# Performance work log

Measured on AMD Instinct MI355X. Metric: run time of the kernel, lower is better.

Reference implementation:

```python
import jax, jax.numpy as jnp
import numpy as np

B, T, E, HD, K, V = 128, 512, 128, 128, 20, 30000  # HD = hidden per direction


def _lstm_dir(x, Wih, Whh, b, reverse):
    # x: [T, B, D]; Wih: [4H, D]; Whh: [4H, H]; b: [4H] (b_ih + b_hh combined)
    if reverse:
        x = x[::-1]
    bsz = x.shape[1]
    xW = jnp.einsum('tbd,gd->tbg', x, Wih) + b  # [T, B, 4H] precompute input proj
    h0 = jnp.zeros((bsz, HD), x.dtype)
    c0 = jnp.zeros((bsz, HD), x.dtype)

    def step(carry, xw):
        h, c = carry
        z = xw + h @ Whh.T
        i, f, g, o = jnp.split(z, 4, axis=-1)  # PyTorch gate order i,f,g,o
        c = jax.nn.sigmoid(f) * c + jax.nn.sigmoid(i) * jnp.tanh(g)
        h = jax.nn.sigmoid(o) * jnp.tanh(c)
        return (h, c), h

    _, hs = jax.lax.scan(step, (h0, c0), xW)
    if reverse:
        hs = hs[::-1]
    return hs


def _bilstm_layer(x, Wih, Whh, b):
    # Wih/Whh: [2, 4H, D]/[2, 4H, H]; b: [2, 4H]
    hf = _lstm_dir(x, Wih[0], Whh[0], b[0], False)
    hb = _lstm_dir(x, Wih[1], Whh[1], b[1], True)
    return jnp.concatenate([hf, hb], axis=-1)  # [T, B, 2H]


def _crf_nll(emissions, tags, trans, start, end):
    # emissions: [B, T, K]; tags: [B, T]; full (all-ones) mask, reduction='mean'
    bsz = emissions.shape[0]
    em_tm = jnp.swapaxes(emissions, 0, 1)  # [T, B, K]
    tags_tm = tags.T                       # [T, B]
    bidx = jnp.arange(bsz)

    # --- numerator: path score ---
    score0 = start[tags_tm[0]] + em_tm[0][bidx, tags_tm[0]]

    def num_step(s, inp):
        em_t, tg_prev, tg_t = inp
        return s + trans[tg_prev, tg_t] + em_t[bidx, tg_t], None

    score, _ = jax.lax.scan(num_step, score0, (em_tm[1:], tags_tm[:-1], tags_tm[1:]))
    score = score + end[tags_tm[-1]]

    # --- denominator: forward algorithm (log partition) ---
    alpha0 = start[None, :] + em_tm[0]  # [B, K]

    def den_step(a, em_t):
        # a[b,i] + trans[i,j] + em_t[b,j] -> logsumexp over i
        a = jax.nn.logsumexp(a[:, :, None] + trans[None], axis=1) + em_t
        return a, None

    alpha, _ = jax.lax.scan(den_step, alpha0, em_tm[1:])
    logZ = jax.nn.logsumexp(alpha + end[None, :], axis=1)

    return -jnp.mean(score - logZ)


def setup_inputs() -> dict:
    key = jax.random.key(0)
    ks = jax.random.split(key, 16)
    u = lambda k, shape, s: jax.random.uniform(k, shape, jnp.float32, -s, s)
    kk = 1.0 / np.sqrt(HD)
    embed = jax.random.normal(ks[0], (V, E), jnp.float32) * 0.1
    embed = embed.at[0].set(0.0)  # padding_idx=0
    inp = {
        'sentences': jax.random.randint(ks[1], (B, T), 1, V),  # no pad tokens -> full mask
        'tags': jax.random.randint(ks[2], (B, T), 0, K),
        'lengths': jnp.full((B,), T, dtype=jnp.int64 if jax.config.jax_enable_x64 else jnp.int32),
        'embed': embed,
        'Wih0': u(ks[3], (2, 4 * HD, E), kk),
        'Whh0': u(ks[4], (2, 4 * HD, HD), kk),
        'b0': u(ks[5], (2, 4 * HD), kk),
        'Wih1': u(ks[6], (2, 4 * HD, 2 * HD), kk),
        'Whh1': u(ks[7], (2, 4 * HD, HD), kk),
        'b1': u(ks[8], (2, 4 * HD), kk),
        'Wout': u(ks[9], (K, 2 * HD), 1.0 / np.sqrt(2 * HD)),
        'bout': u(ks[10], (K,), 1.0 / np.sqrt(2 * HD)),
        'trans': u(ks[11], (K, K), 0.1),
        'start': u(ks[12], (K,), 0.1),
        'end': u(ks[13], (K,), 0.1),
    }
    return inp


def reference(sentences, tags, lengths, embed, Wih0, Whh0, b0, Wih1, Whh1, b1, Wout, bout, trans, start, end):
    # all lengths == T, so pack/pad is identity (eval-mode: no dropout)
    x = embed[sentences]                 # [B, T, E]
    x = jnp.swapaxes(x, 0, 1)            # [T, B, E] time-major for scan
    x = _bilstm_layer(x, Wih0, Whh0, b0)  # [T, B, 2H]
    x = _bilstm_layer(x, Wih1, Whh1, b1)  # [T, B, 2H]
    emissions = jnp.einsum('tbh,kh->tbk', x, Wout) + bout  # [T, B, K]
    emissions = jnp.swapaxes(emissions, 0, 1)              # [B, T, K]
    return _crf_nll(emissions, tags, trans, start, end)
```

## Files before the change

kernel.cpp:

```cpp
#include <hip/hip_runtime.h>
#include <hip/hip_bf16.h>
#include <cstddef>

typedef unsigned short u16;
typedef unsigned int u32;
typedef short bf16x8 __attribute__((ext_vector_type(8)));
typedef unsigned short u16x8 __attribute__((ext_vector_type(8)));
typedef float f32x4 __attribute__((ext_vector_type(4)));
typedef int i32x4 __attribute__((ext_vector_type(4)));
typedef int i32x8 __attribute__((ext_vector_type(8)));

constexpr int CB = 128;
constexpr int CT = 512;
constexpr int CE = 128;
constexpr int CK = 20;

constexpr size_t OFF_FLAG   = 0;
constexpr size_t OFF_WIH0   = 256;
constexpr size_t OFF_WHH0   = OFF_WIH0 + 262144;
constexpr size_t OFF_WIH1   = OFF_WHH0 + 262144;
constexpr size_t OFF_WHH1   = OFF_WIH1 + 524288;
constexpr size_t OFF_WOUT   = OFF_WHH1 + 262144;
constexpr size_t OFF_B0     = OFF_WOUT + 10240;
constexpr size_t OFF_B1     = OFF_B0 + 4096;
constexpr size_t OFF_BOUT   = OFF_B1 + 4096;
constexpr size_t OFF_TRANS  = OFF_BOUT + 256;
constexpr size_t OFF_START  = OFF_TRANS + 1792;
constexpr size_t OFF_END    = OFF_START + 256;
constexpr size_t OFF_PART   = OFF_END + 256;
constexpr size_t OFF_WHH0F8 = OFF_PART + 256;
constexpr size_t OFF_WHH1F8 = OFF_WHH0F8 + 131072;
constexpr size_t OFF_X0     = 2097152;
constexpr size_t OFF_H0     = OFF_X0 + 16777216;
constexpr size_t OFF_H1     = OFF_H0 + 33554432;
constexpr size_t OFF_EM     = OFF_H1 + 33554432;
constexpr size_t OFF_Z      = OFF_EM + 5242880;
constexpr size_t WS_NEED    = OFF_Z + 134217728;

__device__ __forceinline__ float b2f(u16 u) {
    union { u32 i; float f; } v; v.i = ((u32)u) << 16; return v.f;
}
__device__ __forceinline__ u16 f2b(float f) {
    union { float f; u32 i; } v; v.f = f;
    u32 r = v.i + 0x7FFFu + ((v.i >> 16) & 1u);
    return (u16)(r >> 16);
}
__device__ __forceinline__ float ldin(const void* p, long i, int bf) {
    return bf ? b2f(((const u16*)p)[i]) : ((const float*)p)[i];
}
__device__ __forceinline__ float sigm(float x) { return 1.0f / (1.0f + __expf(-x)); }
__device__ __forceinline__ float tanh_f(float x) { return 2.0f / (1.0f + __expf(-2.0f * x)) - 1.0f; }

__device__ __forceinline__ void gload_lds16(const void* g, void* l) {
    __builtin_amdgcn_global_load_lds(
        (const __attribute__((address_space(1))) void*)g,
        (__attribute__((address_space(3))) void*)l, 16, 0, 0);
}

__global__ void sniff_k(const unsigned char* __restrict__ traw, int* __restrict__ flag) {
    int lane = threadIdx.x;
    int votes = 0;
    for (int w = lane; w < 200; w += 64) {
        unsigned char b1 = traw[w * 4 + 1];
        unsigned char e = b1 & 0x7F;
        if (e >= 0x20 && e <= 0x3E) votes++;
    }
    #pragma unroll
    for (int off = 32; off; off >>= 1) votes += __shfl_xor(votes, off);
    if (lane == 0) *flag = (votes > 120) ? 1 : 0;
}

__global__ __launch_bounds__(256) void prep_k(
    const void* wih0, const void* whh0, const void* b0,
    const void* wih1, const void* whh1, const void* b1,
    const void* wout, const void* bout, const void* trans,
    const void* start, const void* end, unsigned char* ws)
{
    const int bf = *(const int*)(ws + OFF_FLAG);
    long tid = (long)blockIdx.x * 256 + threadIdx.x;
    u16* wih0b = (u16*)(ws + OFF_WIH0);
    u16* whh0b = (u16*)(ws + OFF_WHH0);
    u16* wih1b = (u16*)(ws + OFF_WIH1);
    u16* whh1b = (u16*)(ws + OFF_WHH1);
    u16* woutb = (u16*)(ws + OFF_WOUT);
    float* b0f   = (float*)(ws + OFF_B0);
    float* b1f   = (float*)(ws + OFF_B1);
    float* boutf = (float*)(ws + OFF_BOUT);
    float* trf   = (float*)(ws + OFF_TRANS);
    float* stf   = (float*)(ws + OFF_START);
    float* enf   = (float*)(ws + OFF_END);

    if (tid < 131072) { wih0b[tid] = f2b(ldin(wih0, tid, bf)); return; } tid -= 131072;
    if (tid < 131072) { whh0b[tid] = f2b(ldin(whh0, tid, bf)); return; } tid -= 131072;
    if (tid < 1024)   { b0f[tid]   = ldin(b0, tid, bf);        return; } tid -= 1024;
    if (tid < 262144) { wih1b[tid] = f2b(ldin(wih1, tid, bf)); return; } tid -= 262144;
    if (tid < 131072) { whh1b[tid] = f2b(ldin(whh1, tid, bf)); return; } tid -= 131072;
    if (tid < 1024)   { b1f[tid]   = ldin(b1, tid, bf);        return; } tid -= 1024;
    if (tid < 5120)   { woutb[tid] = f2b(ldin(wout, tid, bf)); return; } tid -= 5120;
    if (tid < 20)     { boutf[tid] = ldin(bout, tid, bf);      return; } tid -= 20;
    if (tid < 400)    { trf[tid]   = ldin(trans, tid, bf);     return; } tid -= 400;
    if (tid < 20)     { stf[tid]   = ldin(start, tid, bf);     return; } tid -= 20;
    if (tid < 20)     { enf[tid]   = ldin(end, tid, bf);       return; } tid -= 20;
    if (tid < 65536) {
        const float v0 = ldin(whh0, tid * 2, bf) * 8.0f;
        const float v1 = ldin(whh0, tid * 2 + 1, bf) * 8.0f;
        const u32 pk = __builtin_amdgcn_cvt_pk_fp8_f32(v0, v1, 0, false);
        ((u16*)(ws + OFF_WHH0F8))[tid] = (u16)(pk & 0xFFFF);
        return;
    } tid -= 65536;
    if (tid < 65536) {
        const float v0 = ldin(whh1, tid * 2, bf) * 8.0f;
        const float v1 = ldin(whh1, tid * 2 + 1, bf) * 8.0f;
        const u32 pk = __builtin_amdgcn_cvt_pk_fp8_f32(v0, v1, 0, false);
        ((u16*)(ws + OFF_WHH1F8))[tid] = (u16)(pk & 0xFFFF);
        return;
    }
}

__global__ __launch_bounds__(256) void gather_k(const void* __restrict__ embed,
                                                const int* __restrict__ sent,
                                                unsigned char* __restrict__ ws)
{
    const int bf = *(const int*)(ws + OFF_FLAG);
    u16* x0 = (u16*)(ws + OFF_X0);
    int tid = blockIdx.x * 256 + threadIdx.x;
    int m = tid >> 4, ch = tid & 15;
    int t = m >> 7, b = m & 127;
    int s = sent[b * CT + t];
    long src = (long)s * CE + ch * 8;
    u16x8 o;
    if (bf) {
        o = *(const u16x8*)((const u16*)embed + src);
    } else {
        const float* ef = (const float*)embed + src;
        f32x4 lo = *(const f32x4*)ef;
        f32x4 hi = *(const f32x4*)(ef + 4);
        o[0]=f2b(lo[0]); o[1]=f2b(lo[1]); o[2]=f2b(lo[2]); o[3]=f2b(lo[3]);
        o[4]=f2b(hi[0]); o[5]=f2b(hi[1]); o[6]=f2b(hi[2]); o[7]=f2b(hi[3]);
    }
    *(u16x8*)(x0 + (long)m * CE + ch * 8) = o;
}

template<int KD>
__global__ __launch_bounds__(256) void gemm_k(const u16* __restrict__ A,
                                              const u16* __restrict__ Bw,
                                              const float* __restrict__ bias,
                                              u16* __restrict__ Zp)
{
    const int bid = (blockIdx.x & 7) * 512 + (blockIdx.x >> 3);
    const int bm = bid >> 3, bn = bid & 7;
    const long m0 = (long)bm * 128;
    const int n0 = bn * 128;
    const int tid = threadIdx.x, lane = tid & 63, wave = tid >> 6;
    const int wm = wave >> 1, wn = wave & 1;
    const int lr = lane & 15, kg = (lane >> 4) * 8;

    __shared__ __align__(16) char smem[34816];
    __shared__ float bsm[128];
    u16 (*At)[64] = (u16(*)[64])smem;
    u16 (*Bt)[64] = (u16(*)[64])(smem + 16384);
    u16 (*cho)[136] = (u16(*)[136])smem;
    if (tid < 128) bsm[tid] = bias[n0 + tid];

    f32x4 acc[4][4];
    #pragma unroll
    for (int i = 0; i < 4; ++i)
        #pragma unroll
        for (int j = 0; j < 4; ++j) acc[i][j] = (f32x4){0.f, 0.f, 0.f, 0.f};

    const int srow = tid >> 3, scol = (tid & 7) * 8;
    char* db = smem + (tid & ~63) * 16;
    for (int kk = 0; kk < KD; kk += 64) {
        __syncthreads();
        #pragma unroll
        for (int r = 0; r < 4; ++r)
            gload_lds16(A + (m0 + srow + r * 32) * KD + kk + scol, db + r * 4096);
        #pragma unroll
        for (int r = 0; r < 4; ++r)
            gload_lds16(Bw + (long)(n0 + srow + r * 32) * KD + kk + scol,
                        db + 16384 + r * 4096);
        __syncthreads();
        #pragma unroll
        for (int kh = 0; kh < 64; kh += 32) {
            bf16x8 af[4], bfv[4];
            #pragma unroll
            for (int mt = 0; mt < 4; ++mt)
                af[mt] = *(const bf16x8*)&At[wm * 64 + mt * 16 + lr][kh + kg];
            #pragma unroll
            for (int nt = 0; nt < 4; ++nt)
                bfv[nt] = *(const bf16x8*)&Bt[wn * 64 + nt * 16 + lr][kh + kg];
            #pragma unroll
            for (int mt = 0; mt < 4; ++mt)
                #pragma unroll
                for (int nt = 0; nt < 4; ++nt)
                    acc[mt][nt] = __builtin_amdgcn_mfma_f32_16x16x32_bf16(
                        af[mt], bfv[nt], acc[mt][nt], 0, 0, 0);
        }
    }

    __syncthreads();
    const int rr0 = (lane >> 4) * 4;
    #pragma unroll
    for (int mt = 0; mt < 4; ++mt)
        #pragma unroll
        for (int nt = 0; nt < 4; ++nt) {
            const int colw = wn * 64 + nt * 16 + lr;
            const int pc = (colw >> 5) * 32 + ((colw & 15) << 1) + ((colw >> 4) & 1);
            const float bv = bsm[colw];
            #pragma unroll
            for (int r = 0; r < 4; ++r)
                cho[wm * 64 + mt * 16 + rr0 + r][pc] = f2b(acc[mt][nt][r] + bv);
        }
    __syncthreads();
    const int brow = tid >> 1, hf = tid & 1;
    const int dd = n0 >> 9, gt = (n0 >> 7) & 3;
    const int t = bm;
    const int sz = dd ? (CT - 1 - t) : t;
    u16* dst = Zp + ((long)sz * 256 + (brow * 2 + dd)) * 512 + gt * 128 + hf * 64;
    const u16* srcl = &cho[brow][hf * 64];
    #pragma unroll
    for (int p = 0; p < 8; ++p)
        *(u16x8*)(dst + p * 8) = *(const u16x8*)(srcl + p * 8);
}

__global__ __launch_bounds__(256, 1) void scan_k(const u16* __restrict__ Zp,
                                                 const unsigned char* __restrict__ Whh8,
                                                 u16* __restrict__ hout)
{
    const int b = blockIdx.x & 127, d = blockIdx.x >> 7;
    const int tid = threadIdx.x;
    const int lane = tid & 63;
    const int wave = tid >> 6;
    const int lr = lane & 15;
    const int kb8 = (lane >> 4) * 32;
    const int uhalf = (lane >> 4) & 1;
    const int rowm = wave * 32 + (lane & 31);

    i32x8 bfrag[4][2];
    #pragma unroll
    for (int gt = 0; gt < 4; ++gt)
        #pragma unroll
        for (int uu = 0; uu < 2; ++uu) {
            const unsigned char* wb = Whh8 +
                ((long)(d * 512 + gt * 128 + wave * 32 + uu * 16 + lr) << 7) + kb8;
            const i32x4 lo = *(const i32x4*)wb;
            const i32x4 hi = *(const i32x4*)(wb + 16);
            bfrag[gt][uu] = (i32x8){lo[0], lo[1], lo[2], lo[3], hi[0], hi[1], hi[2], hi[3]};
        }

    __shared__ __align__(16) unsigned char hbuf8[2 * 128];

    constexpr long SLAB = 256 * 256;
    const u32* zw0 = (const u32*)Zp + (long)(b * 2 + d) * 256 + wave * 16 + lr;

    u32 zR[16][4];
    #pragma unroll
    for (int s = 0; s < 16; ++s) {
        #pragma unroll
        for (int g = 0; g < 4; ++g)
            zR[s][g] = zw0[(long)s * SLAB + g * 64];
    }
    const u32* znext = zw0 + 16 * SLAB;

    if (tid < 128) { hbuf8[tid] = 0; hbuf8[128 + tid] = 0; }
    asm volatile("s_waitcnt lgkmcnt(0)\n\ts_barrier" ::: "memory");

    float cst = 0.f;
    u16* hp = hout + ((long)(d ? (CT - 1) : 0) * CB + b) * 256 + d * 128 + rowm;
    const long hstep = (long)(d ? -1 : 1) * (CB * 256);

    for (int grp = 0; grp < 32; ++grp) {
        const bool more = grp < 31;
        #pragma unroll
        for (int slot = 0; slot < 16; ++slot) {
            const u32 zl0 = zR[slot][0], zl1 = zR[slot][1];
            const u32 zl2 = zR[slot][2], zl3 = zR[slot][3];
            if (more) {
                const u32* zp = znext + (long)slot * SLAB;
                zR[slot][0] = zp[0];
                zR[slot][1] = zp[64];
                zR[slot][2] = zp[128];
                zR[slot][3] = zp[192];
            }

            const unsigned char* hbp = hbuf8 + (slot & 1) * 128 + kb8;
            const i32x4 hlo = *(const i32x4*)hbp;
            const i32x4 hhi = *(const i32x4*)(hbp + 16);
            const i32x8 av = (i32x8){hlo[0], hlo[1], hlo[2], hlo[3],
                                     hhi[0], hhi[1], hhi[2], hhi[3]};

            f32x4 acc[4][2];
            #pragma unroll
            for (int gt = 0; gt < 4; ++gt) {
                acc[gt][0] = (f32x4){0.f, 0.f, 0.f, 0.f};
                acc[gt][1] = (f32x4){0.f, 0.f, 0.f, 0.f};
            }
            #pragma unroll
            for (int gt = 0; gt < 4; ++gt) {
                acc[gt][0] = __builtin_amdgcn_mfma_scale_f32_16x16x128_f8f6f4(
                    av, bfrag[gt][0], acc[gt][0], 0, 0,
                    0, 0x7F7F7F7F, 0, 0x7F7F7F7F);
                acc[gt][1] = __builtin_amdgcn_mfma_scale_f32_16x16x128_f8f6f4(
                    av, bfrag[gt][1], acc[gt][1], 0, 0,
                    0, 0x7F7F7F7F, 0, 0x7F7F7F7F);
            }

            const u32 zlw[4] = {zl0, zl1, zl2, zl3};
            float pg[4];
            #pragma unroll
            for (int gt = 0; gt < 4; ++gt) {
                union { u32 i; float f; } zz;
                zz.i = uhalf ? (zlw[gt] & 0xFFFF0000u) : (zlw[gt] << 16);
                const float sv = uhalf ? acc[gt][1][0] : acc[gt][0][0];
                pg[gt] = fmaf(sv, 0.125f, zz.f);
            }
            const float iv = sigm(pg[0]);
            const float fv = sigm(pg[1]);
            const float gg = tanh_f(pg[2]);
            const float ov = sigm(pg[3]);
            cst = fmaf(fv, cst, iv * gg);
            const float h = ov * tanh_f(cst);

            if (lane < 32) {
                const u32 pk = __builtin_amdgcn_cvt_pk_fp8_f32(h, h, 0, false);
                hbuf8[((slot + 1) & 1) * 128 + rowm] = (unsigned char)(pk & 0xFF);
                *hp = f2b(h);
            }
            hp += hstep;
            asm volatile("s_waitcnt lgkmcnt(0)\n\ts_barrier" ::: "memory");
        }
        znext += 16 * SLAB;
    }
}

__global__ __launch_bounds__(256) void emis_k(const u16* __restrict__ h1,
                                              const u16* __restrict__ woutb,
                                              const float* __restrict__ boutf,
                                              float* __restrict__ em)
{
    __shared__ __align__(16) float wsm[CK * 256];
    for (int i = threadIdx.x; i < CK * 256; i += 256) wsm[i] = b2f(woutb[i]);
    __syncthreads();
    const long m = (long)blockIdx.x * 256 + threadIdx.x;
    const u16* hrow = h1 + m * 256;
    float acc[CK];
    #pragma unroll
    for (int n = 0; n < CK; ++n) acc[n] = boutf[n];
    for (int k8 = 0; k8 < 32; ++k8) {
        u16x8 u = *(const u16x8*)(hrow + k8 * 8);
        float hv[8];
        #pragma unroll
        for (int j = 0; j < 8; ++j) hv[j] = b2f(u[j]);
        #pragma unroll
        for (int n = 0; n < CK; ++n) {
            const f32x4 w0 = *(const f32x4*)&wsm[n * 256 + k8 * 8];
            const f32x4 w1 = *(const f32x4*)&wsm[n * 256 + k8 * 8 + 4];
            acc[n] = fmaf(hv[0], w0[0], acc[n]); acc[n] = fmaf(hv[1], w0[1], acc[n]);
            acc[n] = fmaf(hv[2], w0[2], acc[n]); acc[n] = fmaf(hv[3], w0[3], acc[n]);
            acc[n] = fmaf(hv[4], w1[0], acc[n]); acc[n] = fmaf(hv[5], w1[1], acc[n]);
            acc[n] = fmaf(hv[6], w1[2], acc[n]); acc[n] = fmaf(hv[7], w1[3], acc[n]);
        }
    }
    float* emrow = em + m * CK;
    #pragma unroll
    for (int n = 0; n < CK; ++n) emrow[n] = acc[n];
}

__global__ void crf_k(const float* __restrict__ em, const int* __restrict__ tags,
                      const float* __restrict__ trf, const float* __restrict__ stf,
                      const float* __restrict__ enf, float* __restrict__ partial)
{
    const int lane = threadIdx.x;
    if (blockIdx.x < 64) {
        const int j = lane & 31, half = lane >> 5;
        const int b = blockIdx.x * 2 + half;
        const bool act = j < CK;
        float tcol[CK];
        #pragma unroll
        for (int i = 0; i < CK; ++i) tcol[i] = act ? __expf(trf[i * CK + j]) : 0.f;
        float p = act ? __expf(stf[j] + em[(long)b * CK + j]) : 0.f;
        float L = 0.f;
        float emn = act ? em[((long)1 * CB + b) * CK + j] : 0.f;
        for (int t = 1; t < CT; ++t) {
            const float emv = emn;
            if (t + 1 < CT)
                emn = act ? em[((long)(t + 1) * CB + b) * CK + j] : 0.f;
            float pi[CK];
            #pragma unroll
            for (int i = 0; i < CK; ++i) pi[i] = __shfl(p, i, 32);
            float a0 = 0.f, a1 = 0.f, a2 = 0.f, a3 = 0.f;
            #pragma unroll
            for (int i = 0; i < CK; i += 4) {
                a0 = fmaf(pi[i], tcol[i], a0);
                a1 = fmaf(pi[i + 1], tcol[i + 1], a1);
                a2 = fmaf(pi[i + 2], tcol[i + 2], a2);
                a3 = fmaf(pi[i + 3], tcol[i + 3], a3);
            }
            p = ((a0 + a1) + (a2 + a3)) * __expf(emv);
            if ((t & 7) == 0) {
                float sum = act ? p : 0.f;
                #pragma unroll
                for (int off = 16; off; off >>= 1) sum += __shfl_xor(sum, off, 32);
                L += __logf(sum);
                p *= (1.0f / sum);
            }
        }
        float vv = act ? (__logf(p) + L + enf[j]) : -1e30f;
        float mx = vv;
        #pragma unroll
        for (int off = 16; off; off >>= 1) mx = fmaxf(mx, __shfl_xor(mx, off, 32));
        float ex = act ? __expf(vv - mx) : 0.f;
        #pragma unroll
        for (int off = 16; off; off >>= 1) ex += __shfl_xor(ex, off, 32);
        if (j == 0) partial[b] = mx + __logf(ex);
    } else {
        const int b = blockIdx.x - 64;
        float sc = 0.f;
        for (int t = lane; t < CT; t += 64) {
            const int tg = tags[b * CT + t];
            sc += em[((long)t * CB + b) * CK + tg];
            if (t >= 1) sc += trf[tags[b * CT + t - 1] * CK + tg];
        }
        #pragma unroll
        for (int off = 32; off; off >>= 1) sc += __shfl_xor(sc, off);
        if (lane == 0)
            partial[128 + b] = sc + stf[tags[b * CT]] + enf[tags[b * CT + CT - 1]];
    }
}

__global__ void fin_k(const float* __restrict__ partial, void* __restrict__ out,
                      const unsigned char* __restrict__ ws)
{
    const int bf = *(const int*)(ws + OFF_FLAG);
    const int lane = threadIdx.x;
    float v = (partial[lane] - partial[128 + lane]) + (partial[lane + 64] - partial[192 + lane]);
    #pragma unroll
    for (int off = 32; off; off >>= 1) v += __shfl_xor(v, off);
    if (lane == 0) {
        const float mean = v / 128.f;
        if (bf) ((u16*)out)[0] = f2b(mean);
        else    ((float*)out)[0] = mean;
    }
}

extern "C" void kernel_launch(void* const* d_in, const int* in_sizes, int n_in,
                              void* d_out, int out_size, void* d_ws, size_t ws_size,
                              hipStream_t stream) {
    (void)in_sizes; (void)n_in; (void)out_size;
    if (ws_size < WS_NEED) return;
    unsigned char* ws = (unsigned char*)d_ws;

    const void* sent  = d_in[0];
    const void* tags  = d_in[1];
    const void* embed = d_in[3];

    u16* x0  = (u16*)(ws + OFF_X0);
    u16* h0  = (u16*)(ws + OFF_H0);
    u16* h1  = (u16*)(ws + OFF_H1);
    u16* Zb  = (u16*)(ws + OFF_Z);
    float* em = (float*)(ws + OFF_EM);
    float* part = (float*)(ws + OFF_PART);

    sniff_k<<<1, 64, 0, stream>>>((const unsigned char*)d_in[12], (int*)(ws + OFF_FLAG));
    prep_k<<<3102, 256, 0, stream>>>(d_in[4], d_in[5], d_in[6], d_in[7], d_in[8],
                                     d_in[9], d_in[10], d_in[11], d_in[12], d_in[13],
                                     d_in[14], ws);
    gather_k<<<4096, 256, 0, stream>>>(embed, (const int*)sent, ws);
    gemm_k<128><<<4096, 256, 0, stream>>>(x0, (const u16*)(ws + OFF_WIH0),
                                          (const float*)(ws + OFF_B0), Zb);
    scan_k<<<256, 256, 0, stream>>>(Zb, (const unsigned char*)(ws + OFF_WHH0F8), h0);
    gemm_k<256><<<4096, 256, 0, stream>>>(h0, (const u16*)(ws + OFF_WIH1),
                                          (const float*)(ws + OFF_B1), Zb);
    scan_k<<<256, 256, 0, stream>>>(Zb, (const unsigned char*)(ws + OFF_WHH1F8), h1);
    emis_k<<<256, 256, 0, stream>>>(h1, (const u16*)(ws + OFF_WOUT),
                                    (const float*)(ws + OFF_BOUT), em);
    crf_k<<<192, 64, 0, stream>>>(em, (const int*)tags,
                                  (const float*)(ws + OFF_TRANS),
                                  (const float*)(ws + OFF_START),
                                  (const float*)(ws + OFF_END), part);
    fin_k<<<1, 64, 0, stream>>>(part, d_out, ws);
}
```

Baseline: 863.8 us.

## Make input-projection GEMM persistent with resident weight tile and register prefetch

The input-projection GEMM becomes a persistent kernel of 256 blocks. Each block keeps its full 128-column weight slice resident in LDS and loops over 16 M-tiles. The next A tile is prefetched into registers while the current one is computed, LDS uses an XOR swizzle to avoid bank conflicts, and the K loop is fully unrolled over the whole reduction depth. This removes the repeated weight reloads and per-tile launch overhead of the old 4096-block grid, at the cost of lower occupancy (one block per CU with large LDS) and extra barriers per tile.

```diff
diff --git a/kernel.cpp b/kernel.cpp
--- a/kernel.cpp
+++ b/kernel.cpp
@@ -142,53 +142,71 @@
 }
 
 template<int KD>
-__global__ __launch_bounds__(256) void gemm_k(const u16* __restrict__ A,
-                                              const u16* __restrict__ Bw,
-                                              const float* __restrict__ bias,
-                                              u16* __restrict__ Zp)
-{
-    const int bid = (blockIdx.x & 7) * 512 + (blockIdx.x >> 3);
-    const int bm = bid >> 3, bn = bid & 7;
-    const long m0 = (long)bm * 128;
+__global__ __launch_bounds__(256, 1) void gemm_k(const u16* __restrict__ A,
+                                                 const u16* __restrict__ Bw,
+                                                 const float* __restrict__ bias,
+                                                 u16* __restrict__ Zp)
+{
+    constexpr int TB = 128 * KD * 2;
+    constexpr int NI = TB / 4096;
+    constexpr int AR = (TB > 34816) ? TB : 34816;
+    const int bn = blockIdx.x >> 5, mg = blockIdx.x & 31;
     const int n0 = bn * 128;
     const int tid = threadIdx.x, lane = tid & 63, wave = tid >> 6;
     const int wm = wave >> 1, wn = wave & 1;
     const int lr = lane & 15, kg = (lane >> 4) * 8;
 
-    __shared__ __align__(16) char smem[34816];
+    __shared__ __align__(16) char smem[AR + TB];
     __shared__ float bsm[128];
-    u16 (*At)[64] = (u16(*)[64])smem;
-    u16 (*Bt)[64] = (u16(*)[64])(smem + 16384);
+    u16 (*At)[KD] = (u16(*)[KD])smem;
+    u16 (*Bt)[KD] = (u16(*)[KD])(smem + AR);
     u16 (*cho)[136] = (u16(*)[136])smem;
     if (tid < 128) bsm[tid] = bias[n0 + tid];
 
-    f32x4 acc[4][4];
-    #pragma unroll
-    for (int i = 0; i < 4; ++i)
-        #pragma unroll
-        for (int j = 0; j < 4; ++j) acc[i][j] = (f32x4){0.f, 0.f, 0.f, 0.f};
-
-    const int srow = tid >> 3, scol = (tid & 7) * 8;
+    auto swsrc = [&](int p) -> long {
+        const int row = p / (2 * KD);
+        const int sp = (p >> 4) & (KD / 8 - 1);
+        const int sl = sp ^ (row & 7);
+        return (long)row * KD + sl * 8;
+    };
+
     char* db = smem + (tid & ~63) * 16;
-    for (int kk = 0; kk < KD; kk += 64) {
-        __syncthreads();
-        #pragma unroll
-        for (int r = 0; r < 4; ++r)
-            gload_lds16(A + (m0 + srow + r * 32) * KD + kk + scol, db + r * 4096);
-        #pragma unroll
-        for (int r = 0; r < 4; ++r)
-            gload_lds16(Bw + (long)(n0 + srow + r * 32) * KD + kk + scol,
-                        db + 16384 + r * 4096);
-        __syncthreads();
-        #pragma unroll
-        for (int kh = 0; kh < 64; kh += 32) {
+    const u16* Bsrc = Bw + (long)n0 * KD;
+    const u16* Asrc = A + (long)(mg) * 128 * KD;
+    #pragma unroll
+    for (int i = 0; i < NI; ++i)
+        gload_lds16(Bsrc + swsrc(i * 4096 + tid * 16), db + AR + i * 4096);
+    #pragma unroll
+    for (int i = 0; i < NI; ++i)
+        gload_lds16(Asrc + swsrc(i * 4096 + tid * 16), db + i * 4096);
+    __syncthreads();
+
+    u16x8 areg[NI];
+    for (int it = 0; it < 16; ++it) {
+        const int tile = mg + 32 * it;
+        if (it + 1 < 16) {
+            const u16* An = A + (long)(mg + 32 * (it + 1)) * 128 * KD;
+            #pragma unroll
+            for (int i = 0; i < NI; ++i)
+                areg[i] = *(const u16x8*)(An + swsrc(i * 4096 + tid * 16));
+        }
+
+        f32x4 acc[4][4];
+        #pragma unroll
+        for (int i = 0; i < 4; ++i)
+            #pragma unroll
+            for (int j = 0; j < 4; ++j) acc[i][j] = (f32x4){0.f, 0.f, 0.f, 0.f};
+
+        #pragma unroll
+        for (int kt = 0; kt < KD / 32; ++kt) {
+            const int slot = (((kt * 32 + kg) >> 3) ^ (lr & 7)) * 8;
             bf16x8 af[4], bfv[4];
             #pragma unroll
             for (int mt = 0; mt < 4; ++mt)
-                af[mt] = *(const bf16x8*)&At[wm * 64 + mt * 16 + lr][kh + kg];
+                af[mt] = *(const bf16x8*)&At[wm * 64 + mt * 16 + lr][slot];
             #pragma unroll
             for (int nt = 0; nt < 4; ++nt)
-                bfv[nt] = *(const bf16x8*)&Bt[wn * 64 + nt * 16 + lr][kh + kg];
+                bfv[nt] = *(const bf16x8*)&Bt[wn * 64 + nt * 16 + lr][slot];
             #pragma unroll
             for (int mt = 0; mt < 4; ++mt)
                 #pragma unroll
@@ -196,31 +214,37 @@
                     acc[mt][nt] = __builtin_amdgcn_mfma_f32_16x16x32_bf16(
                         af[mt], bfv[nt], acc[mt][nt], 0, 0, 0);
         }
-    }
-
-    __syncthreads();
-    const int rr0 = (lane >> 4) * 4;
-    #pragma unroll
-    for (int mt = 0; mt < 4; ++mt)
-        #pragma unroll
-        for (int nt = 0; nt < 4; ++nt) {
-            const int colw = wn * 64 + nt * 16 + lr;
-            const int pc = (colw >> 5) * 32 + ((colw & 15) << 1) + ((colw >> 4) & 1);
-            const float bv = bsm[colw];
-            #pragma unroll
-            for (int r = 0; r < 4; ++r)
-                cho[wm * 64 + mt * 16 + rr0 + r][pc] = f2b(acc[mt][nt][r] + bv);
-        }
-    __syncthreads();
-    const int brow = tid >> 1, hf = tid & 1;
-    const int dd = n0 >> 9, gt = (n0 >> 7) & 3;
-    const int t = bm;
-    const int sz = dd ? (CT - 1 - t) : t;
-    u16* dst = Zp + ((long)sz * 256 + (brow * 2 + dd)) * 512 + gt * 128 + hf * 64;
-    const u16* srcl = &cho[brow][hf * 64];
-    #pragma unroll
-    for (int p = 0; p < 8; ++p)
-        *(u16x8*)(dst + p * 8) = *(const u16x8*)(srcl + p * 8);
+
+        __syncthreads();
+        const int rr0 = (lane >> 4) * 4;
+        #pragma unroll
+        for (int mt = 0; mt < 4; ++mt)
+            #pragma unroll
+            for (int nt = 0; nt < 4; ++nt) {
+                const int colw = wn * 64 + nt * 16 + lr;
+                const int pc = (colw >> 5) * 32 + ((colw & 15) << 1) + ((colw >> 4) & 1);
+                const float bv = bsm[colw];
+                #pragma unroll
+                for (int r = 0; r < 4; ++r)
+                    cho[wm * 64 + mt * 16 + rr0 + r][pc] = f2b(acc[mt][nt][r] + bv);
+            }
+        __syncthreads();
+        const int brow = tid >> 1, hf = tid & 1;
+        const int dd = n0 >> 9, gt = (n0 >> 7) & 3;
+        const int sz = dd ? (CT - 1 - tile) : tile;
+        u16* dst = Zp + ((long)sz * 256 + (brow * 2 + dd)) * 512 + gt * 128 + hf * 64;
+        const u16* srcl = &cho[brow][hf * 64];
+        #pragma unroll
+        for (int p = 0; p < 8; ++p)
+            *(u16x8*)(dst + p * 8) = *(const u16x8*)(srcl + p * 8);
+        __syncthreads();
+        if (it + 1 < 16) {
+            #pragma unroll
+            for (int i = 0; i < NI; ++i)
+                *(u16x8*)(smem + i * 4096 + tid * 16) = areg[i];
+            __syncthreads();
+        }
+    }
 }
 
 __global__ __launch_bounds__(256, 1) void scan_k(const u16* __restrict__ Zp,
@@ -466,11 +490,11 @@
                                      d_in[9], d_in[10], d_in[11], d_in[12], d_in[13],
                                      d_in[14], ws);
     gather_k<<<4096, 256, 0, stream>>>(embed, (const int*)sent, ws);
-    gemm_k<128><<<4096, 256, 0, stream>>>(x0, (const u16*)(ws + OFF_WIH0),
-                                          (const float*)(ws + OFF_B0), Zb);
+    gemm_k<128><<<256, 256, 0, stream>>>(x0, (const u16*)(ws + OFF_WIH0),
+                                         (const float*)(ws + OFF_B0), Zb);
     scan_k<<<256, 256, 0, stream>>>(Zb, (const unsigned char*)(ws + OFF_WHH0F8), h0);
-    gemm_k<256><<<4096, 256, 0, stream>>>(h0, (const u16*)(ws + OFF_WIH1),
-                                          (const float*)(ws + OFF_B1), Zb);
+    gemm_k<256><<<256, 256, 0, stream>>>(h0, (const u16*)(ws + OFF_WIH1),
+                                         (const float*)(ws + OFF_B1), Zb);
     scan_k<<<256, 256, 0, stream>>>(Zb, (const unsigned char*)(ws + OFF_WHH1F8), h1);
     emis_k<<<256, 256, 0, stream>>>(h1, (const u16*)(ws + OFF_WOUT),
                                     (const float*)(ws + OFF_BOUT), em);
```

Result: no change. 858.7 us (-0.6%).
